# Kernel optimization log

Measured on AMD Instinct MI355X. Metric: run time of the kernel, lower is better.

Reference implementation:

```python
import jax, jax.numpy as jnp
import numpy as np

H, DK, DV, DEMB = 16, 64, 64, 1024
D_MODEL = H * DV


def setup_inputs() -> dict:
    key = jax.random.key(0)
    ks = jax.random.split(key, 9)
    scale = 0.02
    x = jax.random.normal(ks[0], (4, 2048, DEMB), dtype=jnp.float32)
    wq = jax.random.normal(ks[1], (DEMB, H * DK), dtype=jnp.float32) * scale
    bq = jnp.zeros((H * DK,), dtype=jnp.float32)
    wk = jax.random.normal(ks[2], (DEMB, H * DK), dtype=jnp.float32) * scale
    bk = jnp.zeros((H * DK,), dtype=jnp.float32)
    wv = jax.random.normal(ks[3], (DEMB, H * DV), dtype=jnp.float32) * scale
    bv = jnp.zeros((H * DV,), dtype=jnp.float32)
    wo = jax.random.normal(ks[4], (D_MODEL, D_MODEL), dtype=jnp.float32) * scale
    bo = jnp.zeros((D_MODEL,), dtype=jnp.float32)
    return {"x": x, "wq": wq, "bq": bq, "wk": wk, "bk": bk,
            "wv": wv, "bv": bv, "wo": wo, "bo": bo, "mask": 0}


def _split_heads(t, h):
    # (b, s, h*d) -> (b, h, s, d)
    b, s, _ = t.shape
    return t.reshape(b, s, h, -1).transpose(0, 2, 1, 3)


def reference(x, wq, bq, wk, bk, wv, bv, wo, bo, mask):
    b, s, _ = x.shape
    qs = _split_heads(x @ wq + bq, H)  # (b, h, s, dk)
    ks = _split_heads(x @ wk + bk, H)
    vs = _split_heads(x @ wv + bv, H)  # (b, h, s, dv)
    # FAITHFUL quirk: original scales by 1/sqrt(len(ks[0])) == 1/sqrt(n_heads),
    # not 1/sqrt(d_k).
    scores = jnp.einsum('bhqd,bhkd->bhqk', qs, ks) / jnp.sqrt(jnp.float32(H))
    # FAITHFUL quirk: masked_fill(mask == 0, ...) with scalar bool mask is a
    # no-op (True == 0 is False), so no masking is ever applied.
    attn = jax.nn.softmax(scores, axis=-1)
    out = jnp.einsum('bhqk,bhkd->bhqd', attn, vs)  # (b, h, s, dv)
    out = out.transpose(0, 2, 1, 3).reshape(b, s, D_MODEL)
    return out @ wo + bo
```

## Files before the change

### kernel.cpp

```cpp
#include <hip/hip_runtime.h>
#include <stdint.h>

typedef __attribute__((ext_vector_type(8))) short short8;
typedef __attribute__((ext_vector_type(4))) short short4v;
typedef __attribute__((ext_vector_type(4))) float floatx4;
typedef __attribute__((ext_vector_type(4))) _Float16 half4;
typedef __attribute__((ext_vector_type(2))) __fp16 pk2;

#define SEQ 2048
#define NTOK 8192
#define QSCALE 0.360673760222241f

#define MFMA16F16(a,b,c) __builtin_amdgcn_mfma_f32_16x16x16f16((a),(b),(c),0,0,0)

__device__ __forceinline__ float b2f(unsigned short u){
  union { unsigned int i; float f; } v; v.i = ((unsigned int)u) << 16; return v.f;
}
__device__ __forceinline__ unsigned short f2b(float f){
  union { float f; unsigned int i; } v; v.f = f;
  unsigned int r = v.i + 0x7fffu + ((v.i >> 16) & 1u);
  return (unsigned short)(r >> 16);
}
__device__ __forceinline__ void async16(const unsigned short* g, unsigned short* l){
  __builtin_amdgcn_global_load_lds(
      (const __attribute__((address_space(1))) unsigned int*)g,
      (__attribute__((address_space(3))) unsigned int*)l, 16, 0, 0);
}

__global__ __launch_bounds__(256) void prep_kernel(
    const float* __restrict__ x,
    const float* __restrict__ wq, const float* __restrict__ wk,
    const float* __restrict__ wv, const float* __restrict__ wo,
    const float* __restrict__ bq, const float* __restrict__ bk,
    const float* __restrict__ bv,
    unsigned short* __restrict__ xb,
    unsigned short* __restrict__ wqkvT, unsigned short* __restrict__ woT,
    float* __restrict__ bqkv)
{
  __shared__ unsigned short lT[64][72];
  const int bid = blockIdx.x;
  const int tid = threadIdx.x;
  if (bid < 8192){
    int i = (bid*256 + tid)*4;
    float4 v = *(const float4*)(x + i);
    short4v o;
    o[0] = (short)f2b(v.x); o[1] = (short)f2b(v.y);
    o[2] = (short)f2b(v.z); o[3] = (short)f2b(v.w);
    *(short4v*)(xb + i) = o;
  } else if (bid < 9216){
    int idx = bid - 8192;
    int sel = idx >> 8, rest = idx & 255;
    const float* src = (sel==0)?wq:(sel==1)?wk:(sel==2)?wv:wo;
    unsigned short* dst = (sel<3) ? (wqkvT + (size_t)sel*1024*1024) : woT;
    int n0 = (rest & 15) * 64, k0 = (rest >> 4) * 64;
#pragma unroll
    for (int i=0;i<4;i++){
      int ch = tid + i*256;
      int r = ch>>4, c = (ch&15)*4;
      float4 v = *(const float4*)(src + (size_t)(k0+r)*1024 + n0 + c);
      lT[r][c+0] = f2b(v.x); lT[r][c+1] = f2b(v.y);
      lT[r][c+2] = f2b(v.z); lT[r][c+3] = f2b(v.w);
    }
    __syncthreads();
#pragma unroll
    for (int i=0;i<2;i++){
      int ch = tid + i*256;
      int rn = ch>>3, c = (ch&7)*8;
      short8 v;
#pragma unroll
      for (int j=0;j<8;j++) v[j] = (short)lT[c+j][rn];
      *(short8*)(dst + (size_t)(n0+rn)*1024 + k0 + c) = v;
    }
  } else {
    int i = (bid - 9216)*256 + tid;
    if (i < 3072){
      int sel = i >> 10, j = i & 1023;
      bqkv[i] = (sel==0)?bq[j]:(sel==1)?bk[j]:bv[j];
    }
  }
}

template<int MODE>
__global__ __launch_bounds__(256) void gemm_bt_kernel(
    const unsigned short* __restrict__ A,
    const unsigned short* __restrict__ Bt,
    const float* __restrict__ bias,
    void* __restrict__ Cv,
    unsigned short* __restrict__ Vt,
    int M, int N, int K)
{
  __shared__ unsigned short lA[128*64];
  __shared__ unsigned short lB[128*64];
  const int tid  = threadIdx.x;
  const int lane = tid & 63;
  const int wave = tid >> 6;
  const int quad = lane >> 4;
  const int l15  = lane & 15;
  const int wR = (wave >> 1) * 64;
  const int wC = (wave & 1) * 64;
  const int rowB = blockIdx.y * 128;
  const int colB = blockIdx.x * 128;

  const int srow = wave*32 + (lane>>3);
  const int sc8  = (lane&7) ^ (lane>>3);
  const unsigned short* gA = A  + (size_t)(rowB + srow)*K + sc8*8;
  const unsigned short* gB = Bt + (size_t)(colB + srow)*K + sc8*8;
  unsigned short* lAw = lA + wave*32*64 + lane*8;
  unsigned short* lBw = lB + wave*32*64 + lane*8;

  floatx4 acc[4][4];
#pragma unroll
  for (int t=0;t<4;t++)
#pragma unroll
    for (int u=0;u<4;u++) acc[t][u] = (floatx4){0.f,0.f,0.f,0.f};

  for (int kt = 0; kt < K; kt += 64){
    __syncthreads();
#pragma unroll
    for (int i=0;i<4;i++){
      async16(gA + (size_t)i*8*K + kt, lAw + i*512);
      async16(gB + (size_t)i*8*K + kt, lBw + i*512);
    }
    __syncthreads();
#pragma unroll
    for (int ks=0; ks<2; ks++){
      const int cph = ((ks*4 + quad) ^ (l15 & 7)) * 8;
      short8 af[4], bf[4];
#pragma unroll
      for (int t=0;t<4;t++) af[t] = *(const short8*)&lA[(wR + t*16 + l15)*64 + cph];
#pragma unroll
      for (int u=0;u<4;u++) bf[u] = *(const short8*)&lB[(wC + u*16 + l15)*64 + cph];
#pragma unroll
      for (int t=0;t<4;t++)
#pragma unroll
        for (int u=0;u<4;u++)
          acc[t][u] = __builtin_amdgcn_mfma_f32_16x16x32_bf16(af[t], bf[u], acc[t][u], 0, 0, 0);
    }
  }
  if (MODE == 3 && colB >= 2048){
#pragma unroll
    for (int u=0;u<4;u++){
      int col = colB + wC + u*16 + l15;
      float bval = bias[col];
      int vcol = col - 2048;
      int hh = vcol >> 6, dv = vcol & 63;
#pragma unroll
      for (int t=0;t<4;t++){
        int row0 = rowB + wR + t*16 + quad*4;
        int bb = row0 >> 11, s = row0 & 2047;
        union { pk2 p[2]; short4v s4; } cv;
        cv.p[0] = __builtin_amdgcn_cvt_pkrtz(acc[t][u][0]+bval, acc[t][u][1]+bval);
        cv.p[1] = __builtin_amdgcn_cvt_pkrtz(acc[t][u][2]+bval, acc[t][u][3]+bval);
        *(short4v*)(Vt + ((size_t)(bb*16+hh)*64 + dv)*2048 + s) = cv.s4;
      }
    }
  } else {
#pragma unroll
    for (int u=0;u<4;u++){
      int col = colB + wC + u*16 + l15;
      float bval = bias[col];
      float scale = (MODE == 3 && col < 1024) ? QSCALE : 1.0f;
#pragma unroll
      for (int t=0;t<4;t++){
        int row0 = rowB + wR + t*16 + quad*4;
#pragma unroll
        for (int r=0;r<4;r++){
          float val = (acc[t][u][r] + bval) * scale;
          if (MODE == 1) ((float*)Cv)[(size_t)(row0 + r)*N + col] = val;
          else ((unsigned short*)Cv)[(size_t)(row0 + r)*N + col] = f2b(val);
        }
      }
    }
  }
}

__global__ __launch_bounds__(256) void flash_attn_kernel(
    const unsigned short* __restrict__ qkv,
    const unsigned short* __restrict__ vt,
    unsigned short* __restrict__ attn_out)
{
  __shared__ unsigned short sK[2][64][72];
  __shared__ unsigned short sVt[2][64][72];
  const int bh = blockIdx.x;
  const int b = bh >> 4, h = bh & 15;
  const int qt = blockIdx.y;
  const int tid = threadIdx.x;
  const int wave = tid >> 6;
  const int lane = tid & 63;
  const int quad = lane >> 4, l15 = lane & 15;
  const int tok0 = b*SEQ + qt*128;

  short8 qf[2][2];
#pragma unroll
  for (int t=0;t<2;t++)
#pragma unroll
    for (int ks=0;ks<2;ks++)
      qf[t][ks] = *(const short8*)(qkv + (size_t)(tok0 + wave*32 + t*16 + l15)*3072
                                   + h*64 + ks*32 + quad*8);

  floatx4 oacc[2][4];
  float psum[2] = {0.f, 0.f};
#pragma unroll
  for (int t=0;t<2;t++)
#pragma unroll
    for (int v=0;v<4;v++) oacc[t][v] = (floatx4){0.f,0.f,0.f,0.f};

  int R[4], C[4], HF[4], U[4], QD[4];
#pragma unroll
  for (int i=0;i<4;i++){
    int chh = tid + (i&1)*256;
    R[i] = chh >> 3; C[i] = (chh & 7)*8; HF[i] = i >> 1;
    U[i] = C[i] >> 4; QD[i] = (C[i] & 15) >> 2;
  }
  short8 rk[4], rv[4];
#pragma unroll
  for (int i=0;i<4;i++){
    rk[i] = *(const short8*)(qkv + (size_t)(b*SEQ + HF[i]*64 + R[i])*3072 + 1024 + h*64 + C[i]);
    rv[i] = *(const short8*)(vt  + (size_t)(bh*64 + R[i])*2048 + HF[i]*64 + C[i]);
  }

  for (int it = 0; it < SEQ/128; it++){
    __syncthreads();
#pragma unroll
    for (int i=0;i<4;i++){
      *(short8*)&sK[HF[i]][R[i]][C[i]] = rk[i];
      short4v lo = {rv[i][0],rv[i][1],rv[i][2],rv[i][3]};
      short4v hi = {rv[i][4],rv[i][5],rv[i][6],rv[i][7]};
      *(short4v*)&sVt[HF[i]][R[i]][QD[i]*16 + U[i]*4]     = lo;
      *(short4v*)&sVt[HF[i]][R[i]][(QD[i]+1)*16 + U[i]*4] = hi;
    }
    __syncthreads();
    if (it + 1 < SEQ/128){
      int nx = (it + 1) * 128;
#pragma unroll
      for (int i=0;i<4;i++){
        rk[i] = *(const short8*)(qkv + (size_t)(b*SEQ + nx + HF[i]*64 + R[i])*3072 + 1024 + h*64 + C[i]);
        rv[i] = *(const short8*)(vt  + (size_t)(bh*64 + R[i])*2048 + nx + HF[i]*64 + C[i]);
      }
    }

#pragma unroll
    for (int hf=0; hf<2; hf++){
      floatx4 sacc[4][2];
#pragma unroll
      for (int u=0;u<4;u++)
#pragma unroll
        for (int t=0;t<2;t++) sacc[u][t] = (floatx4){0.f,0.f,0.f,0.f};
#pragma unroll
      for (int ks=0;ks<2;ks++){
        short8 kf[4];
#pragma unroll
        for (int u=0;u<4;u++) kf[u] = *(const short8*)&sK[hf][u*16 + l15][ks*32 + quad*8];
#pragma unroll
        for (int u=0;u<4;u++)
#pragma unroll
          for (int t=0;t<2;t++)
            sacc[u][t] = __builtin_amdgcn_mfma_f32_16x16x32_bf16(kf[u], qf[t][ks], sacc[u][t], 0,0,0);
      }

      half4 pf[4][2];
#pragma unroll
      for (int t=0;t<2;t++){
#pragma unroll
        for (int u=0;u<4;u++){
          float p0 = __builtin_amdgcn_exp2f(sacc[u][t][0]);
          float p1 = __builtin_amdgcn_exp2f(sacc[u][t][1]);
          float p2 = __builtin_amdgcn_exp2f(sacc[u][t][2]);
          float p3 = __builtin_amdgcn_exp2f(sacc[u][t][3]);
          psum[t] += (p0+p1)+(p2+p3);
          union { pk2 p2v[2]; half4 h4; } cv;
          cv.p2v[0] = __builtin_amdgcn_cvt_pkrtz(p0,p1);
          cv.p2v[1] = __builtin_amdgcn_cvt_pkrtz(p2,p3);
          pf[u][t] = cv.h4;
        }
      }

#pragma unroll
      for (int v=0;v<4;v++){
        half4 vf[4];
#pragma unroll
        for (int hh=0;hh<2;hh++){
          short8 w = *(const short8*)&sVt[hf][v*16 + l15][quad*16 + hh*8];
          union { short4v s; half4 h; } a, bb;
          a.s  = (short4v){w[0],w[1],w[2],w[3]};
          bb.s = (short4v){w[4],w[5],w[6],w[7]};
          vf[2*hh]   = a.h;
          vf[2*hh+1] = bb.h;
        }
#pragma unroll
        for (int t=0;t<2;t++)
#pragma unroll
          for (int u=0;u<4;u++)
            oacc[t][v] = MFMA16F16(pf[u][t], vf[u], oacc[t][v]);
      }
    }
  }

#pragma unroll
  for (int t=0;t<2;t++){
    float s = psum[t];
    s += __shfl_xor(s, 16);
    s += __shfl_xor(s, 32);
    psum[t] = s;
  }
#pragma unroll
  for (int t=0;t<2;t++){
#pragma unroll
    for (int r=0;r<4;r++){
      float inv = 1.0f / __shfl(psum[t], quad*4 + r);
      int tok = tok0 + wave*32 + t*16 + quad*4 + r;
#pragma unroll
      for (int v=0;v<4;v++)
        attn_out[(size_t)tok*1024 + h*64 + v*16 + l15] = f2b(oacc[t][v][r] * inv);
    }
  }
}

extern "C" void kernel_launch(void* const* d_in, const int* in_sizes, int n_in,
                              void* d_out, int out_size, void* d_ws, size_t ws_size,
                              hipStream_t stream)
{
  const float* x  = (const float*)d_in[0];
  const float* wq = (const float*)d_in[1];
  const float* bq = (const float*)d_in[2];
  const float* wk = (const float*)d_in[3];
  const float* bk = (const float*)d_in[4];
  const float* wv = (const float*)d_in[5];
  const float* bv = (const float*)d_in[6];
  const float* wo = (const float*)d_in[7];
  const float* bo = (const float*)d_in[8];
  float* out = (float*)d_out;

  char* ws = (char*)d_ws;
  unsigned short* wqkvT  = (unsigned short*)(ws);
  unsigned short* woT    = (unsigned short*)(ws + 6291456);
  float*          bqkv   = (float*)(ws + 8388608);
  unsigned short* xb     = (unsigned short*)(ws + 8400896);
  unsigned short* qkvbuf = (unsigned short*)(ws + 25178112);
  unsigned short* vtbuf  = (unsigned short*)(ws + 75509760);
  unsigned short* aobuf  = (unsigned short*)(ws + 92286976);

  prep_kernel<<<dim3(9228), 256, 0, stream>>>(x, wq, wk, wv, wo, bq, bk, bv,
                                              xb, wqkvT, woT, bqkv);
  gemm_bt_kernel<3><<<dim3(24, 64), 256, 0, stream>>>(xb, wqkvT, bqkv, qkvbuf, vtbuf,
                                                      8192, 3072, 1024);
  flash_attn_kernel<<<dim3(64, 16), 256, 0, stream>>>(qkvbuf, vtbuf, aobuf);
  gemm_bt_kernel<1><<<dim3(8, 64), 256, 0, stream>>>(aobuf, woT, bo, out, nullptr,
                                                     8192, 1024, 1024);
}
```

Measured before the change: 290.8 us.

## Use 16x16x32 f16 MFMA for PV with lane-shuffled P fragments and XOR-swizzled LDS

The PV product switches from the 16x16x16 f16 MFMA to the 16x16x32 f16 variant, which halves the number of MFMA instructions. To build the wider A operand, the packed probability registers are rearranged across lanes with xor shuffles. The padded LDS tiles for K and V^T are replaced by unpadded tiles with an XOR swizzle on 16-byte chunks, so stores become single 16-byte writes and bank conflicts are avoided without padding. The cost is extra shuffle and select instructions per tile, and a risk that the register routing does not match the MFMA operand layout.

```diff
diff --git a/kernel.cpp b/kernel.cpp
--- a/kernel.cpp
+++ b/kernel.cpp
@@ -4,14 +4,12 @@
 typedef __attribute__((ext_vector_type(8))) short short8;
 typedef __attribute__((ext_vector_type(4))) short short4v;
 typedef __attribute__((ext_vector_type(4))) float floatx4;
-typedef __attribute__((ext_vector_type(4))) _Float16 half4;
+typedef __attribute__((ext_vector_type(8))) _Float16 half8;
 typedef __attribute__((ext_vector_type(2))) __fp16 pk2;
 
 #define SEQ 2048
 #define NTOK 8192
 #define QSCALE 0.360673760222241f
-
-#define MFMA16F16(a,b,c) __builtin_amdgcn_mfma_f32_16x16x16f16((a),(b),(c),0,0,0)
 
 __device__ __forceinline__ float b2f(unsigned short u){
   union { unsigned int i; float f; } v; v.i = ((unsigned int)u) << 16; return v.f;
@@ -179,8 +177,8 @@
     const unsigned short* __restrict__ vt,
     unsigned short* __restrict__ attn_out)
 {
-  __shared__ unsigned short sK[2][64][72];
-  __shared__ unsigned short sVt[2][64][72];
+  __shared__ __align__(16) unsigned short sK [2][64][64];
+  __shared__ __align__(16) unsigned short sVt[2][64][64];
   const int bh = blockIdx.x;
   const int b = bh >> 4, h = bh & 15;
   const int qt = blockIdx.y;
@@ -188,6 +186,9 @@
   const int wave = tid >> 6;
   const int lane = tid & 63;
   const int quad = lane >> 4, l15 = lane & 15;
+  const bool hi   = quad >= 2;
+  const bool qodd = (quad & 1) != 0;
+  const bool qmid = (quad == 1) | (quad == 2);
   const int tok0 = b*SEQ + qt*128;
 
   short8 qf[2][2];
@@ -205,12 +206,12 @@
 #pragma unroll
     for (int v=0;v<4;v++) oacc[t][v] = (floatx4){0.f,0.f,0.f,0.f};
 
-  int R[4], C[4], HF[4], U[4], QD[4];
+  int R[4], C[4], HF[4], SW[4];
 #pragma unroll
   for (int i=0;i<4;i++){
     int chh = tid + (i&1)*256;
     R[i] = chh >> 3; C[i] = (chh & 7)*8; HF[i] = i >> 1;
-    U[i] = C[i] >> 4; QD[i] = (C[i] & 15) >> 2;
+    SW[i] = (((chh & 7) ^ (R[i] & 7)) * 8);
   }
   short8 rk[4], rv[4];
 #pragma unroll
@@ -219,15 +220,22 @@
     rv[i] = *(const short8*)(vt  + (size_t)(bh*64 + R[i])*2048 + HF[i]*64 + C[i]);
   }
 
+#define ROUTE(Aq, Cq, wlo, whi) {                     \
+    unsigned OWN = hi ? (Cq) : (Aq);                  \
+    unsigned OTH = hi ? (Aq) : (Cq);                  \
+    unsigned XO  = __shfl_xor(OTH, 32);               \
+    unsigned G2  = qmid ? OWN : XO;                   \
+    unsigned H2  = __shfl_xor(G2, 16);                \
+    wlo = qodd ? H2 : (hi ? XO : OWN);                \
+    whi = qodd ? (hi ? OWN : XO) : H2;                \
+  }
+
   for (int it = 0; it < SEQ/128; it++){
     __syncthreads();
 #pragma unroll
     for (int i=0;i<4;i++){
-      *(short8*)&sK[HF[i]][R[i]][C[i]] = rk[i];
-      short4v lo = {rv[i][0],rv[i][1],rv[i][2],rv[i][3]};
-      short4v hi = {rv[i][4],rv[i][5],rv[i][6],rv[i][7]};
-      *(short4v*)&sVt[HF[i]][R[i]][QD[i]*16 + U[i]*4]     = lo;
-      *(short4v*)&sVt[HF[i]][R[i]][(QD[i]+1)*16 + U[i]*4] = hi;
+      *(short8*)&sK [HF[i]][R[i]][SW[i]] = rk[i];
+      *(short8*)&sVt[HF[i]][R[i]][SW[i]] = rv[i];
     }
     __syncthreads();
     if (it + 1 < SEQ/128){
@@ -250,7 +258,8 @@
       for (int ks=0;ks<2;ks++){
         short8 kf[4];
 #pragma unroll
-        for (int u=0;u<4;u++) kf[u] = *(const short8*)&sK[hf][u*16 + l15][ks*32 + quad*8];
+        for (int u=0;u<4;u++)
+          kf[u] = *(const short8*)&sK[hf][u*16 + l15][((ks*4 + quad) ^ (l15 & 7)) * 8];
 #pragma unroll
         for (int u=0;u<4;u++)
 #pragma unroll
@@ -258,7 +267,7 @@
             sacc[u][t] = __builtin_amdgcn_mfma_f32_16x16x32_bf16(kf[u], qf[t][ks], sacc[u][t], 0,0,0);
       }
 
-      half4 pf[4][2];
+      unsigned int pk[4][2][2];
 #pragma unroll
       for (int t=0;t<2;t++){
 #pragma unroll
@@ -268,33 +277,42 @@
           float p2 = __builtin_amdgcn_exp2f(sacc[u][t][2]);
           float p3 = __builtin_amdgcn_exp2f(sacc[u][t][3]);
           psum[t] += (p0+p1)+(p2+p3);
-          union { pk2 p2v[2]; half4 h4; } cv;
-          cv.p2v[0] = __builtin_amdgcn_cvt_pkrtz(p0,p1);
-          cv.p2v[1] = __builtin_amdgcn_cvt_pkrtz(p2,p3);
-          pf[u][t] = cv.h4;
+          union { pk2 p; unsigned u; } c0, c1;
+          c0.p = __builtin_amdgcn_cvt_pkrtz(p0,p1);
+          c1.p = __builtin_amdgcn_cvt_pkrtz(p2,p3);
+          pk[u][t][0] = c0.u; pk[u][t][1] = c1.u;
         }
       }
 
+      half8 af[2][2];
+#pragma unroll
+      for (int t=0;t<2;t++)
+#pragma unroll
+        for (int B=0;B<2;B++){
+          unsigned A0 = pk[2*B][t][0],  A1 = pk[2*B][t][1];
+          unsigned C0 = pk[2*B+1][t][0], C1 = pk[2*B+1][t][1];
+          unsigned w0, w1, w2, w3;
+          ROUTE(A0, C0, w0, w2);
+          ROUTE(A1, C1, w1, w3);
+          union { unsigned u[4]; half8 h; } a;
+          a.u[0]=w0; a.u[1]=w1; a.u[2]=w2; a.u[3]=w3;
+          af[t][B] = a.h;
+        }
+
 #pragma unroll
       for (int v=0;v<4;v++){
-        half4 vf[4];
-#pragma unroll
-        for (int hh=0;hh<2;hh++){
-          short8 w = *(const short8*)&sVt[hf][v*16 + l15][quad*16 + hh*8];
-          union { short4v s; half4 h; } a, bb;
-          a.s  = (short4v){w[0],w[1],w[2],w[3]};
-          bb.s = (short4v){w[4],w[5],w[6],w[7]};
-          vf[2*hh]   = a.h;
-          vf[2*hh+1] = bb.h;
+#pragma unroll
+        for (int B=0;B<2;B++){
+          union { short8 s; half8 h; } vb;
+          vb.s = *(const short8*)&sVt[hf][v*16 + l15][((B*4 + quad) ^ (l15 & 7)) * 8];
+#pragma unroll
+          for (int t=0;t<2;t++)
+            oacc[t][v] = __builtin_amdgcn_mfma_f32_16x16x32_f16(af[t][B], vb.h, oacc[t][v], 0,0,0);
         }
-#pragma unroll
-        for (int t=0;t<2;t++)
-#pragma unroll
-          for (int u=0;u<4;u++)
-            oacc[t][v] = MFMA16F16(pf[u][t], vf[u], oacc[t][v]);
-      }
-    }
-  }
+      }
+    }
+  }
+#undef ROUTE
 
 #pragma unroll
   for (int t=0;t<2;t++){
```

After: 299.9 us. 1.03x slower.
